# Performance work log

Hardware: AMD Instinct MI355X
Metric: run time of the kernel (lower is better)

The kernel has to match this reference:

```python
import jax, jax.numpy as jnp
import numpy as np

EMB = 128
N_LEFT = 100000
N_RIGHT = 100000
N_EDGES = 600000
EDGE_FEAT = 1


def _ortho(key, shape):
    a = jax.random.normal(key, shape, dtype=jnp.float32)
    q, r = jnp.linalg.qr(a if shape[0] >= shape[1] else a.T)
    q = q * jnp.sign(jnp.diag(r))
    return q if shape[0] >= shape[1] else q.T


def setup_inputs() -> dict:
    key = jax.random.key(0)
    ks = jax.random.split(key, 12)
    return {
        "left_features": jax.random.normal(ks[0], (N_LEFT, EMB), dtype=jnp.float32),
        "edge_indices": jax.random.randint(ks[1], (2, N_EDGES), 0, N_LEFT, dtype=jnp.int32).astype(jnp.int64),
        "edge_features": jax.random.normal(ks[2], (N_EDGES, EDGE_FEAT), dtype=jnp.float32),
        "right_features": jax.random.normal(ks[3], (N_RIGHT, EMB), dtype=jnp.float32),
        "scatter_out_size": N_RIGHT,
        # parameters (orthogonal weights, zero biases, unit PreNorm scales)
        "W_left": _ortho(ks[4], (EMB, EMB)),
        "b_left": jnp.zeros((EMB,), jnp.float32),
        "W_edge": _ortho(ks[5], (EMB, EDGE_FEAT)),
        "W_right": _ortho(ks[6], (EMB, EMB)),
        "scale_final": jnp.ones((1,), jnp.float32),
        "W_final": _ortho(ks[7], (EMB, EMB)),
        "b_final": jnp.zeros((EMB,), jnp.float32),
        "scale_post": jnp.ones((1,), jnp.float32),
        "W_out1": _ortho(ks[8], (EMB, 2 * EMB)),
        "b_out1": jnp.zeros((EMB,), jnp.float32),
        "W_out2": _ortho(ks[9], (EMB, EMB)),
        "b_out2": jnp.zeros((EMB,), jnp.float32),
    }


def reference(left_features, edge_indices, edge_features, right_features,
              scatter_out_size, W_left, b_left, W_edge, W_right,
              scale_final, W_final, b_final, scale_post,
              W_out1, b_out1, W_out2, b_out2):
    # node / edge projections
    left_proj = left_features @ W_left.T + b_left            # [n_left, emb]
    edge_proj = edge_features @ W_edge.T                     # [n_edges, emb]
    right_proj = right_features @ W_right.T                  # [n_right, emb]
    # gather per-edge messages and combine
    joint = left_proj[edge_indices[0]] + edge_proj + right_proj[edge_indices[1]]
    # feature_module_final: PreNorm(scale only) -> ReLU -> Linear
    joint = jax.nn.relu(joint * scale_final) @ W_final.T + b_final
    # scatter-add onto right-side nodes (right_to_left=False)
    conv = jax.ops.segment_sum(joint, edge_indices[1], num_segments=scatter_out_size)
    conv = conv * scale_post
    # output MLP on [conv ; prev_right]
    h = jnp.concatenate([conv, right_features], axis=1)      # [n_right, 2*emb]
    h = jax.nn.relu(h @ W_out1.T + b_out1)
    return h @ W_out2.T + b_out2
```

## Files before the change

### kernel.cpp

```cpp
#include <hip/hip_runtime.h>

#define EMB 128

typedef __attribute__((ext_vector_type(8))) short short8;
typedef __attribute__((ext_vector_type(4))) float floatx4;

#define MFMA(a, b, c) __builtin_amdgcn_mfma_f32_16x16x32_bf16((a), (b), (c), 0, 0, 0)

__device__ __forceinline__ ushort f2b(float f) {
    unsigned u = __float_as_uint(f);
    return (ushort)((u + 0x7fff + ((u >> 16) & 1)) >> 16);
}
__device__ __forceinline__ float b2f(ushort h) {
    return __uint_as_float(((unsigned)h) << 16);
}
__device__ __forceinline__ short8 cvt8(const float* p) {
    float4 f0 = *(const float4*)p;
    float4 f1 = *(const float4*)(p + 4);
    short8 v;
    v[0] = f2b(f0.x); v[1] = f2b(f0.y); v[2] = f2b(f0.z); v[3] = f2b(f0.w);
    v[4] = f2b(f1.x); v[5] = f2b(f1.y); v[6] = f2b(f1.z); v[7] = f2b(f1.w);
    return v;
}

__global__ void k_cvt_all(const float* __restrict__ w0, const float* __restrict__ w1,
                          const float* __restrict__ w2, const float* __restrict__ w3,
                          const float* __restrict__ w4, ushort* __restrict__ dst) {
    int i = blockIdx.x * blockDim.x + threadIdx.x;
    const float* src; int off;
    if (i < 16384)      { src = w0; off = i; }
    else if (i < 32768) { src = w1; off = i - 16384; }
    else if (i < 49152) { src = w2; off = i - 32768; }
    else if (i < 81920) { src = w3; off = i - 49152; }
    else                { src = w4; off = i - 81920; }
    dst[i] = f2b(src[off]);
}

__global__ __launch_bounds__(256) void k_proj_mfma(const float* __restrict__ XL,
                                                   const float* __restrict__ XR,
                                                   const ushort* __restrict__ WLb,
                                                   const ushort* __restrict__ WRb,
                                                   const float* __restrict__ bias,
                                                   ushort* __restrict__ YL,
                                                   ushort* __restrict__ YR,
                                                   int n, int nblk) {
    int bid = blockIdx.x;
    const float* X; const ushort* Wb; ushort* Y; int has_bias;
    if (bid < nblk) { X = XL; Wb = WLb; Y = YL; has_bias = 1; }
    else            { X = XR; Wb = WRb; Y = YR; has_bias = 0; bid -= nblk; }

    int t = threadIdx.x, wave = t >> 6, lane = t & 63;
    int m = lane & 15, quad = lane >> 4;
    int rp = (wave & 1) * 32, colg = (wave >> 1) * 64;
    size_t row0 = (size_t)bid * 64;

    short8 a[2][4];
#pragma unroll
    for (int rt = 0; rt < 2; rt++) {
        size_t row = row0 + rp + rt * 16 + m;
        if (row > (size_t)(n - 1)) row = (size_t)(n - 1);
        const float* xr = X + row * EMB;
#pragma unroll
        for (int ks = 0; ks < 4; ks++)
            a[rt][ks] = cvt8(xr + ks * 32 + quad * 8);
    }
#pragma unroll
    for (int ct = 0; ct < 4; ct++) {
        int col = colg + ct * 16 + m;
        floatx4 acc0 = {0.f, 0.f, 0.f, 0.f}, acc1 = {0.f, 0.f, 0.f, 0.f};
#pragma unroll
        for (int ks = 0; ks < 4; ks++) {
            short8 b = *(const short8*)(Wb + (size_t)col * EMB + ks * 32 + quad * 8);
            acc0 = MFMA(a[0][ks], b, acc0);
            acc1 = MFMA(a[1][ks], b, acc1);
        }
        float bb = has_bias ? bias[col] : 0.f;
        size_t r0 = row0 + rp + quad * 4;
#pragma unroll
        for (int r = 0; r < 4; r++) {
            size_t row = r0 + r;
            if (row < (size_t)n) Y[row * EMB + col] = f2b(acc0[r] + bb);
            row += 16;
            if (row < (size_t)n) Y[row * EMB + col] = f2b(acc1[r] + bb);
        }
    }
}

__global__ void k_hist(const int* __restrict__ eidx, int* __restrict__ cnt,
                       int n_edges) {
    int e = blockIdx.x * blockDim.x + threadIdx.x;
    if (e < n_edges) atomicAdd(&cnt[eidx[n_edges + e]], 1);
}

#define SCAN_CHUNK 4096
__global__ __launch_bounds__(1024) void k_scan1(const int* __restrict__ cnt,
                                                int* __restrict__ offs,
                                                int* __restrict__ bsum, int n) {
    __shared__ int buf[1024];
    int t = threadIdx.x;
    int i0 = blockIdx.x * SCAN_CHUNK + t * 4;
    int v[4];
#pragma unroll
    for (int u = 0; u < 4; u++) { int i = i0 + u; v[u] = (i < n) ? cnt[i] : 0; }
    int s = v[0] + v[1] + v[2] + v[3];
    buf[t] = s;
    __syncthreads();
    for (int d = 1; d < 1024; d <<= 1) {
        int x = (t >= d) ? buf[t - d] : 0;
        __syncthreads();
        buf[t] += x;
        __syncthreads();
    }
    int excl = buf[t] - s;
#pragma unroll
    for (int u = 0; u < 4; u++) { int i = i0 + u; if (i < n) offs[i] = excl; excl += v[u]; }
    if (t == 1023) bsum[blockIdx.x] = buf[1023];
}

__global__ __launch_bounds__(1024) void k_scan2(const int* __restrict__ bsum,
                                                int* __restrict__ offs,
                                                int* __restrict__ cursor, int n) {
    int bid = blockIdx.x;
    int base = 0;
    for (int j = 0; j < bid; j++) base += bsum[j];
    int i0 = bid * SCAN_CHUNK + threadIdx.x * 4;
#pragma unroll
    for (int u = 0; u < 4; u++) {
        int i = i0 + u;
        if (i < n) { int o = offs[i] + base; offs[i] = o; cursor[i] = o; }
    }
}

__global__ void k_perm(const int* __restrict__ eidx, const float* __restrict__ ef,
                       int* __restrict__ cursor, int2* __restrict__ sle,
                       int n_edges) {
    int e = blockIdx.x * blockDim.x + threadIdx.x;
    if (e < n_edges) {
        int r = eidx[n_edges + e];
        int p = atomicAdd(&cursor[r], 1);
        int2 v; v.x = eidx[e]; v.y = __float_as_int(ef[e]);
        sle[p] = v;
    }
}

__global__ __launch_bounds__(256) void k_reduce(const ushort* __restrict__ Pl,
                                                const ushort* __restrict__ Pr,
                                                const int2* __restrict__ sle,
                                                const float* __restrict__ We,
                                                const int* __restrict__ offs,
                                                const float* __restrict__ scale_final,
                                                ushort* __restrict__ S,
                                                int n_right, int n_edges) {
    int r = blockIdx.x * 4 + (threadIdx.x >> 6);
    int lane = threadIdx.x & 63;
    float scale = scale_final[0];
    float2 we = *(const float2*)(We + lane * 2);
    ushort2 pru = *(const ushort2*)(Pr + (size_t)r * EMB + lane * 2);
    float prx = b2f(pru.x), pry = b2f(pru.y);
    float ax = 0.f, ay = 0.f;
    int s0 = offs[r];
    int s1 = (r + 1 < n_right) ? offs[r + 1] : n_edges;
    int ei = s0;
    for (; ei + 2 <= s1; ei += 2) {
        int2 e0 = sle[ei], e1 = sle[ei + 1];
        ushort2 p0 = *(const ushort2*)(Pl + (size_t)e0.x * EMB + lane * 2);
        ushort2 p1 = *(const ushort2*)(Pl + (size_t)e1.x * EMB + lane * 2);
        float f0 = __int_as_float(e0.y), f1 = __int_as_float(e1.y);
        ax += fmaxf((b2f(p0.x) + prx + f0 * we.x) * scale, 0.f);
        ay += fmaxf((b2f(p0.y) + pry + f0 * we.y) * scale, 0.f);
        ax += fmaxf((b2f(p1.x) + prx + f1 * we.x) * scale, 0.f);
        ay += fmaxf((b2f(p1.y) + pry + f1 * we.y) * scale, 0.f);
    }
    if (ei < s1) {
        int2 e0 = sle[ei];
        ushort2 p0 = *(const ushort2*)(Pl + (size_t)e0.x * EMB + lane * 2);
        float f0 = __int_as_float(e0.y);
        ax += fmaxf((b2f(p0.x) + prx + f0 * we.x) * scale, 0.f);
        ay += fmaxf((b2f(p0.y) + pry + f0 * we.y) * scale, 0.f);
    }
    ushort2 o; o.x = f2b(ax); o.y = f2b(ay);
    *(ushort2*)(S + (size_t)r * EMB + lane * 2) = o;
}

__global__ __launch_bounds__(256) void k_out_mfma(const ushort* __restrict__ S,
                                                  const float* __restrict__ right,
                                                  const ushort* __restrict__ Wfb,
                                                  const float* __restrict__ bf,
                                                  const int* __restrict__ deg,
                                                  const float* __restrict__ sc_post,
                                                  const ushort* __restrict__ W1b,
                                                  const float* __restrict__ b1,
                                                  const ushort* __restrict__ W2b,
                                                  const float* __restrict__ b2,
                                                  float* __restrict__ out, int n) {
    __shared__ ushort H[64][136];
    __shared__ ushort T[64][136];
    __shared__ float degs[64];
    int t = threadIdx.x, wave = t >> 6, lane = t & 63;
    int m = lane & 15, quad = lane >> 4;
    int rp = (wave & 1) * 32, colg = (wave >> 1) * 64;
    size_t row0 = (size_t)blockIdx.x * 64;
    float sp = sc_post[0];

    if (t < 64) {
        size_t rr = row0 + t;
        degs[t] = (rr < (size_t)n) ? (float)deg[rr] : 0.f;
    }

    short8 a1[2][4], ar[2][4];
#pragma unroll
    for (int rt = 0; rt < 2; rt++) {
        size_t row = row0 + rp + rt * 16 + m;
        if (row > (size_t)(n - 1)) row = (size_t)(n - 1);
        const ushort* sr = S + row * EMB;
        const float* rr = right + row * EMB;
#pragma unroll
        for (int ks = 0; ks < 4; ks++) {
            a1[rt][ks] = *(const short8*)(sr + ks * 32 + quad * 8);
            ar[rt][ks] = cvt8(rr + ks * 32 + quad * 8);
        }
    }
    __syncthreads();

#pragma unroll
    for (int ct = 0; ct < 4; ct++) {
        int col = colg + ct * 16 + m;
        floatx4 acc0 = {0.f, 0.f, 0.f, 0.f}, acc1 = {0.f, 0.f, 0.f, 0.f};
#pragma unroll
        for (int ks = 0; ks < 4; ks++) {
            short8 b = *(const short8*)(Wfb + (size_t)col * EMB + ks * 32 + quad * 8);
            acc0 = MFMA(a1[0][ks], b, acc0);
            acc1 = MFMA(a1[1][ks], b, acc1);
        }
        float bb = bf[col];
        int r0 = rp + quad * 4;
#pragma unroll
        for (int r = 0; r < 4; r++) {
            H[r0 + r][col]      = f2b((acc0[r] + degs[r0 + r] * bb) * sp);
            H[r0 + 16 + r][col] = f2b((acc1[r] + degs[r0 + 16 + r] * bb) * sp);
        }
    }
    __syncthreads();

    short8 a2[2][4];
#pragma unroll
    for (int rt = 0; rt < 2; rt++)
#pragma unroll
        for (int ks = 0; ks < 4; ks++)
            a2[rt][ks] = *(const short8*)(&H[rp + rt * 16 + m][ks * 32 + quad * 8]);
#pragma unroll
    for (int ct = 0; ct < 4; ct++) {
        int col = colg + ct * 16 + m;
        floatx4 acc0 = {0.f, 0.f, 0.f, 0.f}, acc1 = {0.f, 0.f, 0.f, 0.f};
        const ushort* wrow = W1b + (size_t)col * 256;
#pragma unroll
        for (int ks = 0; ks < 4; ks++) {
            short8 b = *(const short8*)(wrow + ks * 32 + quad * 8);
            acc0 = MFMA(a2[0][ks], b, acc0);
            acc1 = MFMA(a2[1][ks], b, acc1);
        }
#pragma unroll
        for (int ks = 0; ks < 4; ks++) {
            short8 b = *(const short8*)(wrow + 128 + ks * 32 + quad * 8);
            acc0 = MFMA(ar[0][ks], b, acc0);
            acc1 = MFMA(ar[1][ks], b, acc1);
        }
        float bb = b1[col];
        int r0 = rp + quad * 4;
#pragma unroll
        for (int r = 0; r < 4; r++) {
            T[r0 + r][col]      = f2b(fmaxf(acc0[r] + bb, 0.f));
            T[r0 + 16 + r][col] = f2b(fmaxf(acc1[r] + bb, 0.f));
        }
    }
    __syncthreads();

    short8 a3[2][4];
#pragma unroll
    for (int rt = 0; rt < 2; rt++)
#pragma unroll
        for (int ks = 0; ks < 4; ks++)
            a3[rt][ks] = *(const short8*)(&T[rp + rt * 16 + m][ks * 32 + quad * 8]);
#pragma unroll
    for (int ct = 0; ct < 4; ct++) {
        int col = colg + ct * 16 + m;
        floatx4 acc0 = {0.f, 0.f, 0.f, 0.f}, acc1 = {0.f, 0.f, 0.f, 0.f};
#pragma unroll
        for (int ks = 0; ks < 4; ks++) {
            short8 b = *(const short8*)(W2b + (size_t)col * EMB + ks * 32 + quad * 8);
            acc0 = MFMA(a3[0][ks], b, acc0);
            acc1 = MFMA(a3[1][ks], b, acc1);
        }
        float bb = b2[col];
        size_t r0 = row0 + rp + quad * 4;
#pragma unroll
        for (int r = 0; r < 4; r++) {
            size_t row = r0 + r;
            if (row < (size_t)n) out[row * EMB + col] = acc0[r] + bb;
            row += 16;
            if (row < (size_t)n) out[row * EMB + col] = acc1[r] + bb;
        }
    }
}

extern "C" void kernel_launch(void* const* d_in, const int* in_sizes, int n_in,
                              void* d_out, int out_size, void* d_ws, size_t ws_size,
                              hipStream_t stream) {
    const float* left   = (const float*)d_in[0];
    const int*   eidx   = (const int*)  d_in[1];
    const float* efeat  = (const float*)d_in[2];
    const float* right  = (const float*)d_in[3];
    const float* W_left = (const float*)d_in[5];
    const float* b_left = (const float*)d_in[6];
    const float* W_edge = (const float*)d_in[7];
    const float* W_right= (const float*)d_in[8];
    const float* sc_fin = (const float*)d_in[9];
    const float* W_fin  = (const float*)d_in[10];
    const float* b_fin  = (const float*)d_in[11];
    const float* sc_post= (const float*)d_in[12];
    const float* W_out1 = (const float*)d_in[13];
    const float* b_out1 = (const float*)d_in[14];
    const float* W_out2 = (const float*)d_in[15];
    const float* b_out2 = (const float*)d_in[16];

    int n_left  = in_sizes[0] / EMB;
    int n_edges = in_sizes[2];
    int n_right = in_sizes[3] / EMB;

    ushort* us = (ushort*)d_ws;
    ushort* Wl_b = us;
    ushort* Wr_b = us + 16384;
    ushort* Wf_b = us + 32768;
    ushort* W1_b = us + 49152;
    ushort* W2_b = us + 81920;
    ushort* Pl   = us + 98304;
    ushort* Pr   = Pl + (size_t)n_left * EMB;
    ushort* S    = Pr + (size_t)n_right * EMB;
    int* cnt    = (int*)(S + (size_t)n_right * EMB);
    int* offs   = cnt + n_right;
    int* cursor = offs + n_right;
    int* bsum   = cursor + n_right;
    int2* sle   = (int2*)(bsum + 64);

    hipMemsetAsync(cnt, 0, (size_t)n_right * sizeof(int), stream);

    k_cvt_all<<<384, 256, 0, stream>>>(W_left, W_right, W_fin, W_out1, W_out2, us);

    int eb = (n_edges + 255) / 256;
    k_hist<<<eb, 256, 0, stream>>>(eidx, cnt, n_edges);
    int nsb = (n_right + SCAN_CHUNK - 1) / SCAN_CHUNK;
    k_scan1<<<nsb, 1024, 0, stream>>>(cnt, offs, bsum, n_right);
    k_scan2<<<nsb, 1024, 0, stream>>>(bsum, offs, cursor, n_right);
    k_perm<<<eb, 256, 0, stream>>>(eidx, efeat, cursor, sle, n_edges);

    int nblk = (n_left + 63) / 64;
    k_proj_mfma<<<2 * nblk, 256, 0, stream>>>(left, right, Wl_b, Wr_b, b_left,
                                              Pl, Pr, n_left, nblk);

    k_reduce<<<n_right / 4, 256, 0, stream>>>(Pl, Pr, sle, W_edge, offs,
                                              sc_fin, S, n_right, n_edges);

    k_out_mfma<<<(n_right + 63) / 64, 256, 0, stream>>>(S, right, Wf_b, b_fin,
                                                        cnt, sc_post, W1_b, b_out1,
                                                        W2_b, b_out2,
                                                        (float*)d_out, n_right);
}
```

Baseline: 411.7 us.

## Fuse right projection, segment reduction and output MLP into one kernel

```diff
diff --git a/kernel.cpp b/kernel.cpp
--- a/kernel.cpp
+++ b/kernel.cpp
@@ -36,23 +36,14 @@
     dst[i] = f2b(src[off]);
 }
 
-__global__ __launch_bounds__(256) void k_proj_mfma(const float* __restrict__ XL,
-                                                   const float* __restrict__ XR,
-                                                   const ushort* __restrict__ WLb,
-                                                   const ushort* __restrict__ WRb,
+__global__ __launch_bounds__(256) void k_proj_left(const float* __restrict__ X,
+                                                   const ushort* __restrict__ Wb,
                                                    const float* __restrict__ bias,
-                                                   ushort* __restrict__ YL,
-                                                   ushort* __restrict__ YR,
-                                                   int n, int nblk) {
-    int bid = blockIdx.x;
-    const float* X; const ushort* Wb; ushort* Y; int has_bias;
-    if (bid < nblk) { X = XL; Wb = WLb; Y = YL; has_bias = 1; }
-    else            { X = XR; Wb = WRb; Y = YR; has_bias = 0; bid -= nblk; }
-
+                                                   ushort* __restrict__ Y, int n) {
     int t = threadIdx.x, wave = t >> 6, lane = t & 63;
     int m = lane & 15, quad = lane >> 4;
     int rp = (wave & 1) * 32, colg = (wave >> 1) * 64;
-    size_t row0 = (size_t)bid * 64;
+    size_t row0 = (size_t)blockIdx.x * 64;
 
     short8 a[2][4];
 #pragma unroll
@@ -74,7 +65,7 @@
             acc0 = MFMA(a[0][ks], b, acc0);
             acc1 = MFMA(a[1][ks], b, acc1);
         }
-        float bb = has_bias ? bias[col] : 0.f;
+        float bb = bias[col];
         size_t r0 = row0 + rp + quad * 4;
 #pragma unroll
         for (int r = 0; r < 4; r++) {
@@ -143,85 +134,120 @@
     }
 }
 
-__global__ __launch_bounds__(256) void k_reduce(const ushort* __restrict__ Pl,
-                                                const ushort* __restrict__ Pr,
-                                                const int2* __restrict__ sle,
-                                                const float* __restrict__ We,
-                                                const int* __restrict__ offs,
-                                                const float* __restrict__ scale_final,
-                                                ushort* __restrict__ S,
-                                                int n_right, int n_edges) {
-    int r = blockIdx.x * 4 + (threadIdx.x >> 6);
-    int lane = threadIdx.x & 63;
-    float scale = scale_final[0];
-    float2 we = *(const float2*)(We + lane * 2);
-    ushort2 pru = *(const ushort2*)(Pr + (size_t)r * EMB + lane * 2);
-    float prx = b2f(pru.x), pry = b2f(pru.y);
-    float ax = 0.f, ay = 0.f;
-    int s0 = offs[r];
-    int s1 = (r + 1 < n_right) ? offs[r + 1] : n_edges;
-    int ei = s0;
-    for (; ei + 2 <= s1; ei += 2) {
-        int2 e0 = sle[ei], e1 = sle[ei + 1];
-        ushort2 p0 = *(const ushort2*)(Pl + (size_t)e0.x * EMB + lane * 2);
-        ushort2 p1 = *(const ushort2*)(Pl + (size_t)e1.x * EMB + lane * 2);
-        float f0 = __int_as_float(e0.y), f1 = __int_as_float(e1.y);
-        ax += fmaxf((b2f(p0.x) + prx + f0 * we.x) * scale, 0.f);
-        ay += fmaxf((b2f(p0.y) + pry + f0 * we.y) * scale, 0.f);
-        ax += fmaxf((b2f(p1.x) + prx + f1 * we.x) * scale, 0.f);
-        ay += fmaxf((b2f(p1.y) + pry + f1 * we.y) * scale, 0.f);
-    }
-    if (ei < s1) {
-        int2 e0 = sle[ei];
-        ushort2 p0 = *(const ushort2*)(Pl + (size_t)e0.x * EMB + lane * 2);
-        float f0 = __int_as_float(e0.y);
-        ax += fmaxf((b2f(p0.x) + prx + f0 * we.x) * scale, 0.f);
-        ay += fmaxf((b2f(p0.y) + pry + f0 * we.y) * scale, 0.f);
-    }
-    ushort2 o; o.x = f2b(ax); o.y = f2b(ay);
-    *(ushort2*)(S + (size_t)r * EMB + lane * 2) = o;
-}
-
-__global__ __launch_bounds__(256) void k_out_mfma(const ushort* __restrict__ S,
-                                                  const float* __restrict__ right,
-                                                  const ushort* __restrict__ Wfb,
-                                                  const float* __restrict__ bf,
-                                                  const int* __restrict__ deg,
-                                                  const float* __restrict__ sc_post,
-                                                  const ushort* __restrict__ W1b,
-                                                  const float* __restrict__ b1,
-                                                  const ushort* __restrict__ W2b,
-                                                  const float* __restrict__ b2,
-                                                  float* __restrict__ out, int n) {
+__global__ __launch_bounds__(256) void k_fused(const float* __restrict__ right,
+                                               const ushort* __restrict__ Wrb,
+                                               const ushort* __restrict__ Pl,
+                                               const int2* __restrict__ sle,
+                                               const float* __restrict__ We,
+                                               const int* __restrict__ offs,
+                                               const float* __restrict__ sc_fin,
+                                               const ushort* __restrict__ Wfb,
+                                               const float* __restrict__ bf,
+                                               const float* __restrict__ sc_post,
+                                               const ushort* __restrict__ W1b,
+                                               const float* __restrict__ b1,
+                                               const ushort* __restrict__ W2b,
+                                               const float* __restrict__ b2,
+                                               float* __restrict__ out,
+                                               int n, int n_edges) {
+    __shared__ ushort PRT[64][136];
+    __shared__ ushort SS[64][136];
     __shared__ ushort H[64][136];
-    __shared__ ushort T[64][136];
     __shared__ float degs[64];
+
     int t = threadIdx.x, wave = t >> 6, lane = t & 63;
     int m = lane & 15, quad = lane >> 4;
     int rp = (wave & 1) * 32, colg = (wave >> 1) * 64;
     size_t row0 = (size_t)blockIdx.x * 64;
+    float scale = sc_fin[0];
     float sp = sc_post[0];
 
     if (t < 64) {
         size_t rr = row0 + t;
-        degs[t] = (rr < (size_t)n) ? (float)deg[rr] : 0.f;
-    }
-
-    short8 a1[2][4], ar[2][4];
+        if (rr < (size_t)n) {
+            int s0 = offs[rr];
+            int s1 = (rr + 1 < (size_t)n) ? offs[rr + 1] : n_edges;
+            degs[t] = (float)(s1 - s0);
+        } else degs[t] = 0.f;
+    }
+
+    short8 ar[2][4];
 #pragma unroll
     for (int rt = 0; rt < 2; rt++) {
         size_t row = row0 + rp + rt * 16 + m;
         if (row > (size_t)(n - 1)) row = (size_t)(n - 1);
-        const ushort* sr = S + row * EMB;
         const float* rr = right + row * EMB;
 #pragma unroll
-        for (int ks = 0; ks < 4; ks++) {
-            a1[rt][ks] = *(const short8*)(sr + ks * 32 + quad * 8);
+        for (int ks = 0; ks < 4; ks++)
             ar[rt][ks] = cvt8(rr + ks * 32 + quad * 8);
-        }
-    }
-    __syncthreads();
-
+    }
+
+#pragma unroll
+    for (int ct = 0; ct < 4; ct++) {
+        int col = colg + ct * 16 + m;
+        floatx4 acc0 = {0.f, 0.f, 0.f, 0.f}, acc1 = {0.f, 0.f, 0.f, 0.f};
+#pragma unroll
+        for (int ks = 0; ks < 4; ks++) {
+            short8 b = *(const short8*)(Wrb + (size_t)col * EMB + ks * 32 + quad * 8);
+            acc0 = MFMA(ar[0][ks], b, acc0);
+            acc1 = MFMA(ar[1][ks], b, acc1);
+        }
+        int r0 = rp + quad * 4;
+#pragma unroll
+        for (int r = 0; r < 4; r++) {
+            PRT[r0 + r][col]      = f2b(acc0[r]);
+            PRT[r0 + 16 + r][col] = f2b(acc1[r]);
+        }
+    }
+    __syncthreads();
+
+    float2 we = *(const float2*)(We + lane * 2);
+    for (int i = 0; i < 16; i++) {
+        int node = wave * 16 + i;
+        size_t grow = row0 + node;
+        float ax = 0.f, ay = 0.f;
+        if (grow < (size_t)n) {
+            int s0 = offs[grow];
+            int s1 = (grow + 1 < (size_t)n) ? offs[grow + 1] : n_edges;
+            ushort2 pru = *(const ushort2*)&PRT[node][lane * 2];
+            float prx = b2f(pru.x), pry = b2f(pru.y);
+            int ei = s0;
+            for (; ei + 4 <= s1; ei += 4) {
+                int2 e0 = sle[ei], e1 = sle[ei + 1], e2 = sle[ei + 2], e3 = sle[ei + 3];
+                ushort2 p0 = *(const ushort2*)(Pl + (size_t)e0.x * EMB + lane * 2);
+                ushort2 p1 = *(const ushort2*)(Pl + (size_t)e1.x * EMB + lane * 2);
+                ushort2 p2 = *(const ushort2*)(Pl + (size_t)e2.x * EMB + lane * 2);
+                ushort2 p3 = *(const ushort2*)(Pl + (size_t)e3.x * EMB + lane * 2);
+                float f0 = __int_as_float(e0.y), f1 = __int_as_float(e1.y);
+                float f2_ = __int_as_float(e2.y), f3 = __int_as_float(e3.y);
+                ax += fmaxf((b2f(p0.x) + prx + f0 * we.x) * scale, 0.f);
+                ay += fmaxf((b2f(p0.y) + pry + f0 * we.y) * scale, 0.f);
+                ax += fmaxf((b2f(p1.x) + prx + f1 * we.x) * scale, 0.f);
+                ay += fmaxf((b2f(p1.y) + pry + f1 * we.y) * scale, 0.f);
+                ax += fmaxf((b2f(p2.x) + prx + f2_ * we.x) * scale, 0.f);
+                ay += fmaxf((b2f(p2.y) + pry + f2_ * we.y) * scale, 0.f);
+                ax += fmaxf((b2f(p3.x) + prx + f3 * we.x) * scale, 0.f);
+                ay += fmaxf((b2f(p3.y) + pry + f3 * we.y) * scale, 0.f);
+            }
+            for (; ei < s1; ei++) {
+                int2 e0 = sle[ei];
+                ushort2 p0 = *(const ushort2*)(Pl + (size_t)e0.x * EMB + lane * 2);
+                float f0 = __int_as_float(e0.y);
+                ax += fmaxf((b2f(p0.x) + prx + f0 * we.x) * scale, 0.f);
+                ay += fmaxf((b2f(p0.y) + pry + f0 * we.y) * scale, 0.f);
+            }
+        }
+        ushort2 o; o.x = f2b(ax); o.y = f2b(ay);
+        *(ushort2*)&SS[node][lane * 2] = o;
+    }
+    __syncthreads();
+
+    short8 a1[2][4];
+#pragma unroll
+    for (int rt = 0; rt < 2; rt++)
+#pragma unroll
+        for (int ks = 0; ks < 4; ks++)
+            a1[rt][ks] = *(const short8*)(&SS[rp + rt * 16 + m][ks * 32 + quad * 8]);
 #pragma unroll
     for (int ct = 0; ct < 4; ct++) {
         int col = colg + ct * 16 + m;
@@ -269,8 +295,8 @@
         int r0 = rp + quad * 4;
 #pragma unroll
         for (int r = 0; r < 4; r++) {
-            T[r0 + r][col]      = f2b(fmaxf(acc0[r] + bb, 0.f));
-            T[r0 + 16 + r][col] = f2b(fmaxf(acc1[r] + bb, 0.f));
+            PRT[r0 + r][col]      = f2b(fmaxf(acc0[r] + bb, 0.f));
+            PRT[r0 + 16 + r][col] = f2b(fmaxf(acc1[r] + bb, 0.f));
         }
     }
     __syncthreads();
@@ -280,7 +306,7 @@
     for (int rt = 0; rt < 2; rt++)
 #pragma unroll
         for (int ks = 0; ks < 4; ks++)
-            a3[rt][ks] = *(const short8*)(&T[rp + rt * 16 + m][ks * 32 + quad * 8]);
+            a3[rt][ks] = *(const short8*)(&PRT[rp + rt * 16 + m][ks * 32 + quad * 8]);
 #pragma unroll
     for (int ct = 0; ct < 4; ct++) {
         int col = colg + ct * 16 + m;
@@ -334,9 +360,7 @@
     ushort* W1_b = us + 49152;
     ushort* W2_b = us + 81920;
     ushort* Pl   = us + 98304;
-    ushort* Pr   = Pl + (size_t)n_left * EMB;
-    ushort* S    = Pr + (size_t)n_right * EMB;
-    int* cnt    = (int*)(S + (size_t)n_right * EMB);
+    int* cnt    = (int*)(Pl + (size_t)n_left * EMB);
     int* offs   = cnt + n_right;
     int* cursor = offs + n_right;
     int* bsum   = cursor + n_right;
@@ -353,15 +377,11 @@
     k_scan2<<<nsb, 1024, 0, stream>>>(bsum, offs, cursor, n_right);
     k_perm<<<eb, 256, 0, stream>>>(eidx, efeat, cursor, sle, n_edges);
 
-    int nblk = (n_left + 63) / 64;
-    k_proj_mfma<<<2 * nblk, 256, 0, stream>>>(left, right, Wl_b, Wr_b, b_left,
-                                              Pl, Pr, n_left, nblk);
-
-    k_reduce<<<n_right / 4, 256, 0, stream>>>(Pl, Pr, sle, W_edge, offs,
-                                              sc_fin, S, n_right, n_edges);
-
-    k_out_mfma<<<(n_right + 63) / 64, 256, 0, stream>>>(S, right, Wf_b, b_fin,
-                                                        cnt, sc_post, W1_b, b_out1,
-                                                        W2_b, b_out2,
-                                                        (float*)d_out, n_right);
-}
+    k_proj_left<<<(n_left + 63) / 64, 256, 0, stream>>>(left, Wl_b, b_left, Pl, n_left);
+
+    k_fused<<<(n_right + 63) / 64, 256, 0, stream>>>(right, Wr_b, Pl, sle, W_edge,
+                                                     offs, sc_fin, Wf_b, b_fin,
+                                                     sc_post, W1_b, b_out1,
+                                                     W2_b, b_out2,
+                                                     (float*)d_out, n_right, n_edges);
+}
```

Result: slower. 429.3 us (+4.3%).
